# Kernel optimization log

Measured on AMD Instinct MI355X. Metric: run time of the kernel, lower is better.

Reference implementation:

```python
import jax, jax.numpy as jnp
import numpy as np

EPS_NORM = 1e-8
EPS_Q = 1e-5

def rmsnorm(x, g):
    var = jnp.mean(x * x, axis=-1, keepdims=True)
    return x * jax.lax.rsqrt(var + EPS_NORM) * g

def activation_quant(x):
    # per-token int8 absmax quantization
    scale = 127.0 / jnp.clip(jnp.max(jnp.abs(x), axis=-1, keepdims=True), EPS_Q, None)
    return jnp.clip(jnp.round(x * scale), -128.0, 127.0) / scale

def weight_quant(w):
    # per-tensor ternary absmean quantization
    scale = 1.0 / jnp.clip(jnp.mean(jnp.abs(w)), EPS_Q, None)
    return jnp.clip(jnp.round(w * scale), -1.0, 1.0) / scale

def ste(x, qfn):
    # straight-through estimator: forward quantized, backward identity
    return x + jax.lax.stop_gradient(qfn(x) - x)

def bitlinear(x, w, g):
    h = rmsnorm(x, g)
    hq = ste(h, activation_quant)
    wq = ste(w, weight_quant)
    return jnp.einsum('bsh,oh->bso', hq, wq)

def setup_inputs() -> dict:
    key = jax.random.key(0)
    k1, k2, k3 = jax.random.split(key, 3)
    B, S, H = 2, 2048, 2048
    I = int(H * 4.0)  # intermediate_size = 8192
    x = jax.random.normal(k1, (B, S, H), dtype=jnp.float32)
    w_gate = jax.random.normal(k2, (2 * I, H), dtype=jnp.float32) * 0.02
    g_gate = jnp.ones((H,), dtype=jnp.float32)
    w_down = jax.random.normal(k3, (H, I), dtype=jnp.float32) * 0.02
    g_down = jnp.ones((I,), dtype=jnp.float32)
    return {"x": x, "w_gate": w_gate, "g_gate": g_gate, "w_down": w_down, "g_down": g_down}

def reference(x, w_gate, g_gate, w_down, g_down):
    y = bitlinear(x, w_gate, g_gate)        # [B,S,2I]
    gate, up = jnp.split(y, 2, axis=-1)     # each [B,S,I]
    z = bitlinear(jax.nn.silu(gate) * up, w_down, g_down)  # [B,S,H]
    return z
```

## Files before the change

kernel.cpp:

```cpp
#include <hip/hip_runtime.h>
#include <hip/hip_bf16.h>
#include <hip/hip_fp16.h>

#define DEVINL __device__ __forceinline__

typedef float f32x4 __attribute__((ext_vector_type(4)));
typedef int i32x4 __attribute__((ext_vector_type(4)));
typedef unsigned int u32x4 __attribute__((ext_vector_type(4)));
typedef unsigned int u32x2 __attribute__((ext_vector_type(2)));

typedef __attribute__((address_space(1))) void void_g;
typedef __attribute__((address_space(3))) void void_l;

DEVINL void gload16(const void* g, void* l) {
  __builtin_amdgcn_global_load_lds((void_g*)g, (void_l*)l, 16, 0, 0);
}

DEVINL float wave_sum(float v) {
  #pragma unroll
  for (int o = 32; o > 0; o >>= 1) v += __shfl_down(v, o, 64);
  return v;
}
DEVINL float wave_max(float v) {
  #pragma unroll
  for (int o = 32; o > 0; o >>= 1) v = fmaxf(v, __shfl_down(v, o, 64));
  return v;
}

DEVINL unsigned int pack4(float a, float b, float c, float d) {
  return ((unsigned int)(unsigned char)(signed char)(int)a)
       | (((unsigned int)(unsigned char)(signed char)(int)b) << 8)
       | (((unsigned int)(unsigned char)(signed char)(int)c) << 16)
       | (((unsigned int)(unsigned char)(signed char)(int)d) << 24);
}

__global__ __launch_bounds__(256) void absum_kernel(const float* __restrict__ w,
                                                    long long nchunk, double* __restrict__ out) {
  long long stride = (long long)gridDim.x * 256;
  long long i = (long long)blockIdx.x * 256 + threadIdx.x;
  float s = 0.f;
  for (; i < nchunk; i += stride) {
    f32x4 v = ((const f32x4*)w)[i];
    s += fabsf(v[0]) + fabsf(v[1]) + fabsf(v[2]) + fabsf(v[3]);
  }
  s = wave_sum(s);
  __shared__ float red[4];
  int lane = threadIdx.x & 63, wv = threadIdx.x >> 6;
  if (lane == 0) red[wv] = s;
  __syncthreads();
  if (threadIdx.x == 0) atomicAdd(out, (double)(red[0] + red[1] + red[2] + red[3]));
}

__global__ __launch_bounds__(256) void quantw_kernel(const float* __restrict__ w,
                                                     signed char* __restrict__ tern,
                                                     long long nchunk,
                                                     const double* __restrict__ sum, double inv_n) {
  float scale = (float)(1.0 / fmax(*sum * inv_n, 1e-5));
  long long stride = (long long)gridDim.x * 256;
  long long i = (long long)blockIdx.x * 256 + threadIdx.x;
  for (; i < nchunk; i += stride) {
    f32x4 v0 = ((const f32x4*)w)[2 * i];
    f32x4 v1 = ((const f32x4*)w)[2 * i + 1];
    float t[8];
    #pragma unroll
    for (int k = 0; k < 4; k++) {
      t[k]     = fminf(fmaxf(rintf(v0[k] * scale), -1.f), 1.f);
      t[4 + k] = fminf(fmaxf(rintf(v1[k] * scale), -1.f), 1.f);
    }
    u32x2 o;
    o[0] = pack4(t[0], t[1], t[2], t[3]);
    o[1] = pack4(t[4], t[5], t[6], t[7]);
    ((u32x2*)tern)[i] = o;
  }
}

__global__ __launch_bounds__(256) void actq1_kernel(const float* __restrict__ x,
                                                    const float* __restrict__ g,
                                                    signed char* __restrict__ q,
                                                    float* __restrict__ a) {
  int t = blockIdx.x, tid = threadIdx.x;
  int lane = tid & 63, wv = tid >> 6;
  __shared__ float redS[4], redM[4];

  const f32x4* xr = (const f32x4*)(x + (size_t)t * 2048);
  f32x4 v0 = xr[tid * 2], v1 = xr[tid * 2 + 1];
  float ssq = 0.f;
  #pragma unroll
  for (int k = 0; k < 4; k++) ssq += v0[k] * v0[k] + v1[k] * v1[k];
  float ws_ = wave_sum(ssq);
  if (lane == 0) redS[wv] = ws_;
  __syncthreads();
  float tot = redS[0] + redS[1] + redS[2] + redS[3];
  float r = rsqrtf(tot / 2048.f + 1e-8f);

  f32x4 g0 = ((const f32x4*)g)[tid * 2], g1 = ((const f32x4*)g)[tid * 2 + 1];
  float h[8], amax = 0.f;
  #pragma unroll
  for (int k = 0; k < 4; k++) {
    h[k]     = v0[k] * r * g0[k];
    h[4 + k] = v1[k] * r * g1[k];
    amax = fmaxf(amax, fmaxf(fabsf(h[k]), fabsf(h[4 + k])));
  }
  float wm = wave_max(amax);
  if (lane == 0) redM[wv] = wm;
  __syncthreads();
  float am = fmaxf(fmaxf(fmaxf(redM[0], redM[1]), fmaxf(redM[2], redM[3])), 1e-5f);
  float scale = 127.f / am;

  float qv[8];
  #pragma unroll
  for (int k = 0; k < 8; k++) qv[k] = fminf(fmaxf(rintf(h[k] * scale), -128.f), 127.f);
  u32x2 o;
  o[0] = pack4(qv[0], qv[1], qv[2], qv[3]);
  o[1] = pack4(qv[4], qv[5], qv[6], qv[7]);
  ((u32x2*)(q + (size_t)t * 2048))[tid] = o;
  if (tid == 0) a[t] = am / 127.f;
}

__global__ __launch_bounds__(256) void silu_rms_q_kernel(const unsigned short* __restrict__ y,
                                                         const float* __restrict__ g,
                                                         signed char* __restrict__ q2,
                                                         float* __restrict__ a2) {
  int t = blockIdx.x, tid = threadIdx.x;
  int lane = tid & 63, wv = tid >> 6;
  __shared__ float redS[4], redM[4];
  const u32x4* gate = (const u32x4*)(y + (size_t)t * 16384);
  const u32x4* up   = (const u32x4*)(y + (size_t)t * 16384 + 8192);

  float v[32];
  float ssq = 0.f;
  #pragma unroll
  for (int b = 0; b < 4; b++) {
    u32x4 gr = gate[b * 256 + tid];
    u32x4 ur = up[b * 256 + tid];
    #pragma unroll
    for (int k = 0; k < 4; k++) {
      float g0 = __half2float(__ushort_as_half((unsigned short)(gr[k] & 0xFFFFu)));
      float g1 = __half2float(__ushort_as_half((unsigned short)(gr[k] >> 16)));
      float u0 = __half2float(__ushort_as_half((unsigned short)(ur[k] & 0xFFFFu)));
      float u1 = __half2float(__ushort_as_half((unsigned short)(ur[k] >> 16)));
      float v0 = g0 / (1.f + expf(-g0)) * u0;
      float v1 = g1 / (1.f + expf(-g1)) * u1;
      v[b * 8 + 2 * k] = v0;
      v[b * 8 + 2 * k + 1] = v1;
      ssq += v0 * v0 + v1 * v1;
    }
  }
  float ws_ = wave_sum(ssq);
  if (lane == 0) redS[wv] = ws_;
  __syncthreads();
  float tot = redS[0] + redS[1] + redS[2] + redS[3];
  float r = rsqrtf(tot / 8192.f + 1e-8f);

  float amax = 0.f;
  #pragma unroll
  for (int b = 0; b < 4; b++) {
    f32x4 ga = ((const f32x4*)g)[b * 512 + tid * 2];
    f32x4 gb = ((const f32x4*)g)[b * 512 + tid * 2 + 1];
    #pragma unroll
    for (int k = 0; k < 4; k++) {
      float h0 = v[b * 8 + k]     * r * ga[k];
      float h1 = v[b * 8 + 4 + k] * r * gb[k];
      v[b * 8 + k] = h0;
      v[b * 8 + 4 + k] = h1;
      amax = fmaxf(amax, fmaxf(fabsf(h0), fabsf(h1)));
    }
  }
  float wm = wave_max(amax);
  if (lane == 0) redM[wv] = wm;
  __syncthreads();
  float am = fmaxf(fmaxf(fmaxf(redM[0], redM[1]), fmaxf(redM[2], redM[3])), 1e-5f);
  float scale = 127.f / am;

  #pragma unroll
  for (int b = 0; b < 4; b++) {
    float qv[8];
    #pragma unroll
    for (int k = 0; k < 8; k++)
      qv[k] = fminf(fmaxf(rintf(v[b * 8 + k] * scale), -128.f), 127.f);
    u32x2 o;
    o[0] = pack4(qv[0], qv[1], qv[2], qv[3]);
    o[1] = pack4(qv[4], qv[5], qv[6], qv[7]);
    ((u32x2*)(q2 + (size_t)t * 8192))[b * 256 + tid] = o;
  }
  if (tid == 0) a2[t] = am / 127.f;
}

template <int OUT_MODE>
__global__ __launch_bounds__(256) void gemm_i8_kernel(const signed char* __restrict__ A,
                                                      const signed char* __restrict__ B,
                                                      void* __restrict__ Cv,
                                                      int M, int N, int K,
                                                      const float* __restrict__ rowscale,
                                                      const double* __restrict__ wsum, double inv_n) {
  __shared__ signed char As[8192];
  __shared__ signed char Bs[8192];
  const int tid = threadIdx.x;
  const int lane = tid & 63;
  const int wv = tid >> 6;
  const int wm = wv >> 1, wn = wv & 1;
  const int m0 = blockIdx.y * 128;
  const int n0 = blockIdx.x * 128;

  const int rr = tid >> 2;
  const int cc = (tid & 3) * 16;
  const signed char* Ag0 = A + (size_t)(m0 + rr) * K + cc;
  const signed char* Ag1 = A + (size_t)(m0 + 64 + rr) * K + cc;
  const signed char* Bg0 = B + (size_t)(n0 + rr) * K + cc;
  const signed char* Bg1 = B + (size_t)(n0 + 64 + rr) * K + cc;
  signed char* lA0 = &As[tid * 16];
  signed char* lA1 = &As[4096 + tid * 16];
  signed char* lB0 = &Bs[tid * 16];
  signed char* lB1 = &Bs[4096 + tid * 16];

  i32x4 acc[4][4] = {};

  const int fr = (lane & 15);
  const int kof = (lane >> 4) * 16;

  for (int k0 = 0; k0 < K; k0 += 64) {
    gload16(Ag0 + k0, lA0);
    gload16(Ag1 + k0, lA1);
    gload16(Bg0 + k0, lB0);
    gload16(Bg1 + k0, lB1);
    __syncthreads();
    i32x4 af[4], bfr[4];
    #pragma unroll
    for (int i = 0; i < 4; i++)
      af[i] = *(const i32x4*)&As[(wm * 64 + i * 16 + fr) * 64 + kof];
    #pragma unroll
    for (int j = 0; j < 4; j++)
      bfr[j] = *(const i32x4*)&Bs[(wn * 64 + j * 16 + fr) * 64 + kof];
    #pragma unroll
    for (int i = 0; i < 4; i++)
      #pragma unroll
      for (int j = 0; j < 4; j++)
        acc[i][j] = __builtin_amdgcn_mfma_i32_16x16x64_i8(af[i], bfr[j], acc[i][j], 0, 0, 0);
    __syncthreads();
  }

  float sw = (float)fmax(*wsum * inv_n, 1e-5);
  const int q = lane >> 4;
  const int cbase = n0 + wn * 64 + (lane & 15);
  #pragma unroll
  for (int i = 0; i < 4; i++) {
    int rowb = m0 + wm * 64 + i * 16 + q * 4;
    #pragma unroll
    for (int r = 0; r < 4; r++) {
      float sc = rowscale[rowb + r] * sw;
      size_t off = (size_t)(rowb + r) * N + cbase;
      #pragma unroll
      for (int j = 0; j < 4; j++) {
        float vv = (float)acc[i][j][r] * sc;
        if (OUT_MODE == 0) ((unsigned short*)Cv)[off + j * 16] = __half_as_ushort(__float2half(vv));
        else               ((float*)Cv)[off + j * 16] = vv;
      }
    }
  }
}

extern "C" void kernel_launch(void* const* d_in, const int* in_sizes, int n_in,
                              void* d_out, int out_size, void* d_ws, size_t ws_size,
                              hipStream_t stream) {
  const float* x      = (const float*)d_in[0];
  const float* w_gate = (const float*)d_in[1];
  const float* g_gate = (const float*)d_in[2];
  const float* w_down = (const float*)d_in[3];
  const float* g_down = (const float*)d_in[4];
  float* out = (float*)d_out;

  char* ws = (char*)d_ws;
  double* sums = (double*)ws;
  float* a1 = (float*)(ws + 4096);
  float* a2 = (float*)(ws + 20480);
  const size_t MB = 1024 * 1024;
  signed char* tern_g = (signed char*)(ws + 65536);
  signed char* q2     = tern_g;
  signed char* tern_d = (signed char*)(ws + 65536 + 32 * MB);
  signed char* q1     = (signed char*)(ws + 65536 + 48 * MB);
  unsigned short* yh  = (unsigned short*)(ws + 65536 + 56 * MB);

  hipMemsetAsync(sums, 0, 16, stream);
  absum_kernel<<<2048, 256, 0, stream>>>(w_gate, 33554432LL / 4, sums + 0);
  absum_kernel<<<1024, 256, 0, stream>>>(w_down, 16777216LL / 4, sums + 1);
  quantw_kernel<<<4096, 256, 0, stream>>>(w_gate, tern_g, 33554432LL / 8, sums + 0, 1.0 / 33554432.0);
  quantw_kernel<<<2048, 256, 0, stream>>>(w_down, tern_d, 16777216LL / 8, sums + 1, 1.0 / 16777216.0);
  actq1_kernel<<<4096, 256, 0, stream>>>(x, g_gate, q1, a1);
  gemm_i8_kernel<0><<<dim3(128, 32), 256, 0, stream>>>(q1, tern_g, yh, 4096, 16384, 2048,
                                                       a1, sums + 0, 1.0 / 33554432.0);
  silu_rms_q_kernel<<<4096, 256, 0, stream>>>(yh, g_down, q2, a2);
  gemm_i8_kernel<1><<<dim3(16, 32), 256, 0, stream>>>(q2, tern_d, out, 4096, 2048, 8192,
                                                      a2, sums + 1, 1.0 / 16777216.0);
}
```

Before: 657.4 us.

## Switch int8 GEMM to 32x32x32 MFMA with 128-deep K tiles

Replaces the 16x16x64 int8 MFMA tiling with 32x32x32 instructions (2x2 per wave) and doubles the K-step to 128, so shared memory per operand grows to 16KB. Fewer LDS fragment loads per MFMA and half as many barrier pairs per K are meant to raise MFMA utilization. The epilogue is remapped to the 32x32 accumulator layout. Row stride of 128 bytes in LDS may cause more bank conflicts, and the larger LDS footprint could lower occupancy.

Result: slower. 773.8 us (+17.7%).

```diff
diff --git a/kernel.cpp b/kernel.cpp
--- a/kernel.cpp
+++ b/kernel.cpp
@@ -6,6 +6,7 @@
 
 typedef float f32x4 __attribute__((ext_vector_type(4)));
 typedef int i32x4 __attribute__((ext_vector_type(4)));
+typedef int i32x16 __attribute__((ext_vector_type(16)));
 typedef unsigned int u32x4 __attribute__((ext_vector_type(4)));
 typedef unsigned int u32x2 __attribute__((ext_vector_type(2)));
 
@@ -193,8 +194,8 @@
                                                       int M, int N, int K,
                                                       const float* __restrict__ rowscale,
                                                       const double* __restrict__ wsum, double inv_n) {
-  __shared__ signed char As[8192];
-  __shared__ signed char Bs[8192];
+  __shared__ signed char As[16384];
+  __shared__ signed char Bs[16384];
   const int tid = threadIdx.x;
   const int lane = tid & 63;
   const int wv = tid >> 6;
@@ -202,58 +203,60 @@
   const int m0 = blockIdx.y * 128;
   const int n0 = blockIdx.x * 128;
 
-  const int rr = tid >> 2;
-  const int cc = (tid & 3) * 16;
-  const signed char* Ag0 = A + (size_t)(m0 + rr) * K + cc;
-  const signed char* Ag1 = A + (size_t)(m0 + 64 + rr) * K + cc;
-  const signed char* Bg0 = B + (size_t)(n0 + rr) * K + cc;
-  const signed char* Bg1 = B + (size_t)(n0 + 64 + rr) * K + cc;
-  signed char* lA0 = &As[tid * 16];
-  signed char* lA1 = &As[4096 + tid * 16];
-  signed char* lB0 = &Bs[tid * 16];
-  signed char* lB1 = &Bs[4096 + tid * 16];
-
-  i32x4 acc[4][4] = {};
-
-  const int fr = (lane & 15);
-  const int kof = (lane >> 4) * 16;
-
-  for (int k0 = 0; k0 < K; k0 += 64) {
-    gload16(Ag0 + k0, lA0);
-    gload16(Ag1 + k0, lA1);
-    gload16(Bg0 + k0, lB0);
-    gload16(Bg1 + k0, lB1);
+  const int srow = tid >> 3;
+  const int scol = (tid & 7) * 16;
+  const signed char* Ag = A + (size_t)(m0 + srow) * K + scol;
+  const signed char* Bg = B + (size_t)(n0 + srow) * K + scol;
+  signed char* ldA = &As[tid * 16];
+  signed char* ldB = &Bs[tid * 16];
+
+  i32x16 acc[2][2] = {};
+
+  const int lrow = lane & 31;
+  const int lhalf = lane >> 5;
+  const signed char* aB = &As[(wm * 64 + lrow) * 128 + lhalf * 16];
+  const signed char* bB = &Bs[(wn * 64 + lrow) * 128 + lhalf * 16];
+
+  const size_t g32K = (size_t)32 * K;
+  for (int k0 = 0; k0 < K; k0 += 128) {
+    #pragma unroll
+    for (int g = 0; g < 4; g++) {
+      gload16(Ag + g * g32K + k0, ldA + g * 4096);
+      gload16(Bg + g * g32K + k0, ldB + g * 4096);
+    }
     __syncthreads();
-    i32x4 af[4], bfr[4];
-    #pragma unroll
-    for (int i = 0; i < 4; i++)
-      af[i] = *(const i32x4*)&As[(wm * 64 + i * 16 + fr) * 64 + kof];
-    #pragma unroll
-    for (int j = 0; j < 4; j++)
-      bfr[j] = *(const i32x4*)&Bs[(wn * 64 + j * 16 + fr) * 64 + kof];
-    #pragma unroll
-    for (int i = 0; i < 4; i++)
-      #pragma unroll
-      for (int j = 0; j < 4; j++)
-        acc[i][j] = __builtin_amdgcn_mfma_i32_16x16x64_i8(af[i], bfr[j], acc[i][j], 0, 0, 0);
+    #pragma unroll
+    for (int c = 0; c < 4; c++) {
+      i32x4 a0 = *(const i32x4*)(aB + c * 32);
+      i32x4 a1 = *(const i32x4*)(aB + 32 * 128 + c * 32);
+      i32x4 b0 = *(const i32x4*)(bB + c * 32);
+      i32x4 b1 = *(const i32x4*)(bB + 32 * 128 + c * 32);
+      acc[0][0] = __builtin_amdgcn_mfma_i32_32x32x32_i8(a0, b0, acc[0][0], 0, 0, 0);
+      acc[0][1] = __builtin_amdgcn_mfma_i32_32x32x32_i8(a0, b1, acc[0][1], 0, 0, 0);
+      acc[1][0] = __builtin_amdgcn_mfma_i32_32x32x32_i8(a1, b0, acc[1][0], 0, 0, 0);
+      acc[1][1] = __builtin_amdgcn_mfma_i32_32x32x32_i8(a1, b1, acc[1][1], 0, 0, 0);
+    }
     __syncthreads();
   }
 
   float sw = (float)fmax(*wsum * inv_n, 1e-5);
-  const int q = lane >> 4;
-  const int cbase = n0 + wn * 64 + (lane & 15);
-  #pragma unroll
-  for (int i = 0; i < 4; i++) {
-    int rowb = m0 + wm * 64 + i * 16 + q * 4;
-    #pragma unroll
-    for (int r = 0; r < 4; r++) {
-      float sc = rowscale[rowb + r] * sw;
-      size_t off = (size_t)(rowb + r) * N + cbase;
-      #pragma unroll
-      for (int j = 0; j < 4; j++) {
-        float vv = (float)acc[i][j][r] * sc;
-        if (OUT_MODE == 0) ((unsigned short*)Cv)[off + j * 16] = __half_as_ushort(__float2half(vv));
-        else               ((float*)Cv)[off + j * 16] = vv;
+  const int cbase = n0 + wn * 64 + lrow;
+  #pragma unroll
+  for (int it = 0; it < 2; it++) {
+    int rbase = m0 + wm * 64 + it * 32 + 4 * lhalf;
+    #pragma unroll
+    for (int reg = 0; reg < 16; reg++) {
+      int row = rbase + (reg & 3) + 8 * (reg >> 2);
+      float sc = rowscale[row] * sw;
+      size_t off = (size_t)row * N + cbase;
+      float v0 = (float)acc[it][0][reg] * sc;
+      float v1 = (float)acc[it][1][reg] * sc;
+      if (OUT_MODE == 0) {
+        ((unsigned short*)Cv)[off]      = __half_as_ushort(__float2half(v0));
+        ((unsigned short*)Cv)[off + 32] = __half_as_ushort(__float2half(v1));
+      } else {
+        ((float*)Cv)[off]      = v0;
+        ((float*)Cv)[off + 32] = v1;
       }
     }
   }
```
